# Kernel tuning notes

Hardware: AMD Instinct MI355X
Metric: run time of the kernel (lower is better)

## Reference

```python
import jax, jax.numpy as jnp
import numpy as np

B, NLAY, NX, NXS, NY, NYS, H = 16384, 60, 4, 3, 4, 3, 128


def _lstm(x, h0, c0, Wih, Whh, bih, bhh):
    """torch-style single-layer LSTM (gate order i,f,g,o). x: [B,T,F] -> ([B,T,H], hN, cN)."""
    xs = jnp.swapaxes(x, 0, 1)  # [T,B,F]
    b = bih + bhh

    def step(carry, xt):
        h, c = carry
        z = xt @ Wih.T + h @ Whh.T + b  # [B,4H]
        i, f, g, o = jnp.split(z, 4, axis=-1)
        c = jax.nn.sigmoid(f) * c + jax.nn.sigmoid(i) * jnp.tanh(g)
        h = jax.nn.sigmoid(o) * jnp.tanh(c)
        return (h, c), h

    (hN, cN), hs = jax.lax.scan(step, (h0, c0), xs)
    return jnp.swapaxes(hs, 0, 1), hN, cN


def setup_inputs() -> dict:
    key = jax.random.key(0)
    ks = jax.random.split(key, 23)
    p = lambda k, s: jax.random.normal(k, s, jnp.float32) * 0.05
    nx_rnn1 = NX + H  # nx + nh_mem (memory='Hidden')
    return {
        "inputs_main": jax.random.normal(ks[0], (B, NLAY, NX), jnp.float32),
        "inputs_sfc": jax.random.normal(ks[1], (B, NXS), jnp.float32),
        "rnn1_mem0": jax.random.normal(ks[2], (B, NLAY, H), jnp.float32),
        "hx2": jax.random.normal(ks[3], (B, H), jnp.float32),
        "cx2": jax.random.normal(ks[4], (B, H), jnp.float32),
        "Ws1": p(ks[5], (H, NXS)), "bs1": p(ks[6], (H,)),
        "Ws2": p(ks[7], (H, NXS)), "bs2": p(ks[8], (H,)),
        "Wih1": p(ks[9], (4 * H, nx_rnn1)), "Whh1": p(ks[10], (4 * H, H)),
        "bih1": p(ks[11], (4 * H,)), "bhh1": p(ks[12], (4 * H,)),
        "Wih2": p(ks[13], (4 * H, H)), "Whh2": p(ks[14], (4 * H, H)),
        "bih2": p(ks[15], (4 * H,)), "bhh2": p(ks[16], (4 * H,)),
        "Wlat": p(ks[17], (H, H)), "blat": p(ks[18], (H,)),
        "Wout": p(ks[19], (NY, H)), "bout": p(ks[20], (NY,)),
        "Wsfc": p(ks[21], (NYS, H)), "bsfc": p(ks[22], (NYS,)),
    }


def reference(inputs_main, inputs_sfc, rnn1_mem0, hx2, cx2,
              Ws1, bs1, Ws2, bs2,
              Wih1, Whh1, bih1, bhh1,
              Wih2, Whh2, bih2, bhh2,
              Wlat, blat, Wout, bout, Wsfc, bsfc):
    # initial states for rnn1 from surface features (random_init_cx=False)
    hx = jnp.tanh(inputs_sfc @ Ws1.T + bs1)
    cx = jnp.tanh(inputs_sfc @ Ws2.T + bs2)
    # flip vertical axis (TOA->surface ordering), append hidden memory
    x_flip = inputs_main[:, ::-1, :]
    rnn1_in = jnp.concatenate([x_flip, rnn1_mem0], axis=2)  # [B,NLAY,NX+H]
    r1, _, _ = _lstm(rnn1_in, hx, cx, Wih1, Whh1, bih1, bhh1)
    r1 = r1[:, ::-1, :]  # flip back
    # second LSTM with (externally supplied) random initial states
    r2, hN, _ = _lstm(r1, hx2, cx2, Wih2, Whh2, bih2, bhh2)
    # intermediate mlp + output head (use_intermediate_mlp=True, concat=False)
    lat = r2 @ Wlat.T + blat  # [B,NLAY,H]
    out = lat @ Wout.T + bout  # [B,NLAY,NY]
    out_sfc = hN @ Wsfc.T + bsfc  # [B,NYS]
    return out, out_sfc
```

## Files before the change

### kernel.cpp

```cpp
#include <hip/hip_runtime.h>

#define B_ 16384
#define T_ 60
#define H_ 128
#define LDST 296

typedef unsigned short u16;
typedef short bf16x8 __attribute__((ext_vector_type(8)));
typedef float f32x4 __attribute__((ext_vector_type(4)));

__device__ __forceinline__ u16 f2bf(float f) {
  union { float f; unsigned int u; } v; v.f = f;
  unsigned int r = v.u + 0x7fffu + ((v.u >> 16) & 1u);
  return (u16)(r >> 16);
}
__device__ __forceinline__ float bf2f(u16 b) {
  union { unsigned int u; float f; } v; v.u = ((unsigned int)b) << 16;
  return v.f;
}
__device__ __forceinline__ float sigm(float x) {
  return __builtin_amdgcn_rcpf(1.f + __expf(-x));
}
__device__ __forceinline__ float tanh_f(float x) {
  return 1.f - 2.f * __builtin_amdgcn_rcpf(1.f + __expf(2.f * x));
}

__global__ void prep_kernel(const float* __restrict__ Wih1, const float* __restrict__ Whh1,
                            const float* __restrict__ Wih2, const float* __restrict__ Whh2,
                            const float* __restrict__ Wlat, const float* __restrict__ blat,
                            const float* __restrict__ Wout, const float* __restrict__ bout,
                            u16* __restrict__ wfrag1, u16* __restrict__ wfrag2,
                            float* __restrict__ Wco, float* __restrict__ bco) {
  const int N1 = 9 * 32 * 64;
  const int N2 = 8 * 32 * 64;
  const int total = N1 + N2 + 512 + 4;
  for (int idx = blockIdx.x * blockDim.x + threadIdx.x; idx < total;
       idx += gridDim.x * blockDim.x) {
    if (idx < N1) {
      int c = idx >> 11;
      int rem = idx & 2047;
      int nt = rem >> 6, lane = rem & 63;
      int n = nt * 16 + (lane & 15);
      int kb = c * 32 + (lane >> 4) * 8;
      u16* dst = wfrag1 + (size_t)idx * 8;
      for (int jj = 0; jj < 8; ++jj) {
        int k = kb + jj;
        float x;
        if (k < 128)      x = Wih1[n * 132 + 4 + k];
        else if (k < 256) x = Whh1[n * 128 + (k - 128)];
        else if (k < 260) x = Wih1[n * 132 + (k - 256)];
        else              x = 0.f;
        dst[jj] = f2bf(x);
      }
    } else if (idx < N1 + N2) {
      int i2 = idx - N1;
      int c = i2 >> 11;
      int rem = i2 & 2047;
      int nt = rem >> 6, lane = rem & 63;
      int n = nt * 16 + (lane & 15);
      int kb = c * 32 + (lane >> 4) * 8;
      u16* dst = wfrag2 + (size_t)i2 * 8;
      for (int jj = 0; jj < 8; ++jj) {
        int k = kb + jj;
        float x = (k < 128) ? Wih2[n * 128 + k] : Whh2[n * 128 + (k - 128)];
        dst[jj] = f2bf(x);
      }
    } else if (idx < N1 + N2 + 512) {
      int i = idx - (N1 + N2);
      int y = i >> 7, k = i & 127;
      float acc = 0.f;
      for (int j = 0; j < 128; ++j) acc = fmaf(Wout[y * 128 + j], Wlat[j * 128 + k], acc);
      Wco[i] = acc;
    } else {
      int y = idx - (N1 + N2 + 512);
      float acc = bout[y];
      for (int j = 0; j < 128; ++j) acc = fmaf(Wout[y * 128 + j], blat[j], acc);
      bco[y] = acc;
    }
  }
}

template <int NC>
__device__ __forceinline__ void do_mfma(const u16* __restrict__ As,
                                        const u16* __restrict__ wfrag,
                                        int w, int lane, f32x4 acc[4][4]) {
  const int lr = lane & 15, lq = lane >> 4;
  const u16* ab = As + lr * LDST + lq * 8;
  const u16* bb = wfrag + (size_t)(w * 512 + lane * 8);
  bf16x8 bcur[4];
#pragma unroll
  for (int g = 0; g < 4; ++g) bcur[g] = *(const bf16x8*)(bb + g * 4096);
#pragma unroll
  for (int c = 0; c < NC; ++c) {
    bf16x8 bnxt[4];
    const int cn = (c + 1 < NC) ? c + 1 : c;
#pragma unroll
    for (int g = 0; g < 4; ++g)
      bnxt[g] = *(const bf16x8*)(bb + (size_t)cn * 16384 + g * 4096);
    bf16x8 af[4];
#pragma unroll
    for (int mt = 0; mt < 4; ++mt)
      af[mt] = *(const bf16x8*)(ab + mt * (16 * LDST) + c * 32);
#pragma unroll
    for (int g = 0; g < 4; ++g)
#pragma unroll
      for (int mt = 0; mt < 4; ++mt)
        acc[mt][g] = __builtin_amdgcn_mfma_f32_16x16x32_bf16(af[mt], bcur[g], acc[mt][g], 0, 0, 0);
#pragma unroll
    for (int g = 0; g < 4; ++g) bcur[g] = bnxt[g];
  }
}

__device__ __forceinline__ void cell_update(f32x4 acc[4][4], float4 bz,
                                            float* __restrict__ cr, u16* __restrict__ hb) {
#pragma unroll
  for (int mt = 0; mt < 4; ++mt)
#pragma unroll
    for (int r = 0; r < 4; ++r) {
      int idx = mt * 4 + r;
      float gi = sigm(acc[mt][0][r] + bz.x);
      float gf = sigm(acc[mt][1][r] + bz.y);
      float gg = tanh_f(acc[mt][2][r] + bz.z);
      float go = sigm(acc[mt][3][r] + bz.w);
      float c = gf * cr[idx] + gi * gg;
      cr[idx] = c;
      hb[idx] = f2bf(go * tanh_f(c));
    }
}

__device__ __forceinline__ float dot8w(uint4 hu, const float* __restrict__ wp, float a) {
  const unsigned* h = (const unsigned*)&hu;
#pragma unroll
  for (int i = 0; i < 4; ++i) {
    union { unsigned u; float f; } hl, hh;
    hl.u = h[i] << 16; hh.u = h[i] & 0xffff0000u;
    a = fmaf(hl.f, wp[2 * i], a);
    a = fmaf(hh.f, wp[2 * i + 1], a);
  }
  return a;
}

__global__ __launch_bounds__(512, 2) void rnn_persist(
    const float* __restrict__ inputs_main, const float* __restrict__ inputs_sfc,
    const float* __restrict__ rnn1_mem0, const float* __restrict__ hx2,
    const float* __restrict__ cx2,
    const float* __restrict__ Ws1, const float* __restrict__ bs1,
    const float* __restrict__ Ws2, const float* __restrict__ bs2,
    const float* __restrict__ bih1, const float* __restrict__ bhh1,
    const float* __restrict__ bih2, const float* __restrict__ bhh2,
    const float* __restrict__ Wsfc, const float* __restrict__ bsfc,
    const u16* __restrict__ wfrag1, const u16* __restrict__ wfrag2,
    const float* __restrict__ Wco, const float* __restrict__ bco,
    u16* __restrict__ r1buf, float* __restrict__ out, float* __restrict__ out_sfc) {
  __shared__ __align__(16) u16 As[64 * LDST];
  __shared__ __align__(16) float WcoS[4 * 132];
  __shared__ __align__(16) float WsfcS[3 * 132];

  const int tid = threadIdx.x;
  const int w = tid >> 6, lane = tid & 63, lr = lane & 15, lq = lane >> 4;
  const int jg = w * 16 + lr;
  const size_t row0 = (size_t)blockIdx.x * 64;

  const float4 bz1 = make_float4(bih1[jg] + bhh1[jg], bih1[128 + jg] + bhh1[128 + jg],
                                 bih1[256 + jg] + bhh1[256 + jg], bih1[384 + jg] + bhh1[384 + jg]);
  const float4 bz2 = make_float4(bih2[jg] + bhh2[jg], bih2[128 + jg] + bhh2[128 + jg],
                                 bih2[256 + jg] + bhh2[256 + jg], bih2[384 + jg] + bhh2[384 + jg]);
  const float bcoy = bco[tid & 3];

  if (tid < 512) WcoS[(tid >> 7) * 132 + (tid & 127)] = Wco[tid];
  if (tid < 384) WsfcS[(tid >> 7) * 132 + (tid & 127)] = Wsfc[tid];

#pragma unroll
  for (int kk = 0; kk < 4; ++kk) {
    int f = tid + kk * 512;
    As[(f >> 5) * LDST + 256 + (f & 31)] = 0;
  }

  float cr[16];
  u16 hb[16];
  {
    float w1a = Ws1[jg * 3], w1b = Ws1[jg * 3 + 1], w1c = Ws1[jg * 3 + 2], b1 = bs1[jg];
    float w2a = Ws2[jg * 3], w2b = Ws2[jg * 3 + 1], w2c = Ws2[jg * 3 + 2], b2 = bs2[jg];
#pragma unroll
    for (int mt = 0; mt < 4; ++mt)
#pragma unroll
      for (int r = 0; r < 4; ++r) {
        int rl = mt * 16 + lq * 4 + r;
        const float* sp = inputs_sfc + (row0 + rl) * 3;
        float s0 = sp[0], s1 = sp[1], s2 = sp[2];
        float h0 = tanh_f(fmaf(s2, w1c, fmaf(s1, w1b, fmaf(s0, w1a, b1))));
        cr[mt * 4 + r] = tanh_f(fmaf(s2, w2c, fmaf(s1, w2b, fmaf(s0, w2a, b2))));
        As[rl * LDST + 128 + jg] = f2bf(h0);
      }
  }
#pragma unroll
  for (int kk = 0; kk < 4; ++kk) {
    int f = tid + kk * 512, row = f >> 5, i = f & 31;
    float4 v = *(const float4*)(rnn1_mem0 + (row0 + row) * (T_ * H_) + i * 4);
    *(ushort4*)&As[row * LDST + i * 4] =
        make_ushort4(f2bf(v.x), f2bf(v.y), f2bf(v.z), f2bf(v.w));
  }
  if (tid < 64) {
    float4 v = *(const float4*)(inputs_main + ((row0 + tid) * T_ + 59) * 4);
    *(ushort4*)&As[tid * LDST + 256] = make_ushort4(f2bf(v.x), f2bf(v.y), f2bf(v.z), f2bf(v.w));
  }
  __syncthreads();

#pragma unroll 1
  for (int s = 0; s < T_; ++s) {
    const int sn = (s < 59) ? s + 1 : 59;
    float4 mv[4];
#pragma unroll
    for (int kk = 0; kk < 4; ++kk) {
      int f = tid + kk * 512;
      mv[kk] = *(const float4*)(rnn1_mem0 + (row0 + (f >> 5)) * (T_ * H_) + sn * 128 + (f & 31) * 4);
    }
    float4 xv = make_float4(0, 0, 0, 0);
    if (tid < 64) xv = *(const float4*)(inputs_main + ((row0 + tid) * T_ + (59 - sn)) * 4);

    f32x4 acc[4][4];
#pragma unroll
    for (int mt = 0; mt < 4; ++mt)
#pragma unroll
      for (int g = 0; g < 4; ++g) acc[mt][g] = (f32x4){0.f, 0.f, 0.f, 0.f};
    do_mfma<9>(As, wfrag1, w, lane, acc);
    cell_update(acc, bz1, cr, hb);
#pragma unroll
    for (int mt = 0; mt < 4; ++mt)
#pragma unroll
      for (int r = 0; r < 4; ++r)
        r1buf[((size_t)s * B_ + row0 + mt * 16 + lq * 4 + r) * H_ + jg] = hb[mt * 4 + r];
    __syncthreads();
#pragma unroll
    for (int mt = 0; mt < 4; ++mt)
#pragma unroll
      for (int r = 0; r < 4; ++r)
        As[(mt * 16 + lq * 4 + r) * LDST + 128 + jg] = hb[mt * 4 + r];
#pragma unroll
    for (int kk = 0; kk < 4; ++kk) {
      int f = tid + kk * 512, row = f >> 5, i = f & 31;
      *(ushort4*)&As[row * LDST + i * 4] =
          make_ushort4(f2bf(mv[kk].x), f2bf(mv[kk].y), f2bf(mv[kk].z), f2bf(mv[kk].w));
    }
    if (tid < 64)
      *(ushort4*)&As[tid * LDST + 256] = make_ushort4(f2bf(xv.x), f2bf(xv.y), f2bf(xv.z), f2bf(xv.w));
    __syncthreads();
  }

  {
    uint4 cv[2];
#pragma unroll
    for (int kk = 0; kk < 2; ++kk) {
      int f = tid + kk * 512;
      cv[kk] = *(const uint4*)&As[(f >> 4) * LDST + 128 + (f & 15) * 8];
    }
    __syncthreads();
#pragma unroll
    for (int kk = 0; kk < 2; ++kk) {
      int f = tid + kk * 512;
      *(uint4*)&As[(f >> 4) * LDST + (f & 15) * 8] = cv[kk];
    }
#pragma unroll
    for (int mt = 0; mt < 4; ++mt)
#pragma unroll
      for (int r = 0; r < 4; ++r) {
        int rl = mt * 16 + lq * 4 + r;
        size_t gi = (row0 + rl) * H_ + jg;
        cr[mt * 4 + r] = cx2[gi];
        As[rl * LDST + 128 + jg] = f2bf(hx2[gi]);
      }
    __syncthreads();
  }

#pragma unroll 1
  for (int t = 0; t < T_; ++t) {
    const int slabn = (t < 59) ? (58 - t) : 0;
    uint4 rv[2];
#pragma unroll
    for (int kk = 0; kk < 2; ++kk) {
      int f = tid + kk * 512;
      rv[kk] = *(const uint4*)(r1buf + ((size_t)slabn * B_ + row0 + (f >> 4)) * H_ + (f & 15) * 8);
    }
    f32x4 acc[4][4];
#pragma unroll
    for (int mt = 0; mt < 4; ++mt)
#pragma unroll
      for (int g = 0; g < 4; ++g) acc[mt][g] = (f32x4){0.f, 0.f, 0.f, 0.f};
    do_mfma<8>(As, wfrag2, w, lane, acc);
    cell_update(acc, bz2, cr, hb);
    __syncthreads();
#pragma unroll
    for (int mt = 0; mt < 4; ++mt)
#pragma unroll
      for (int r = 0; r < 4; ++r)
        As[(mt * 16 + lq * 4 + r) * LDST + 128 + jg] = hb[mt * 4 + r];
#pragma unroll
    for (int kk = 0; kk < 2; ++kk) {
      int f = tid + kk * 512;
      *(uint4*)&As[(f >> 4) * LDST + (f & 15) * 8] = rv[kk];
    }
    __syncthreads();
    if (tid < 256) {
      int row = tid >> 2, y = tid & 3;
      float a = bcoy;
      const u16* hrow = As + row * LDST + 128;
      const float* wrow = WcoS + y * 132;
#pragma unroll
      for (int sg = 0; sg < 16; ++sg)
        a = dot8w(*(const uint4*)(hrow + sg * 8), wrow + sg * 8, a);
      out[((row0 + row) * T_ + t) * 4 + y] = a;
    }
    if (t == 59 && tid >= 256) {
      int q = tid - 256;
      int row = q >> 2, y = q & 3;
      if (y < 3) {
        float a = bsfc[y];
        const u16* hrow = As + row * LDST + 128;
        const float* wrow = WsfcS + y * 132;
#pragma unroll
        for (int sg = 0; sg < 16; ++sg)
          a = dot8w(*(const uint4*)(hrow + sg * 8), wrow + sg * 8, a);
        out_sfc[(row0 + row) * 3 + y] = a;
      }
    }
  }
}

extern "C" void kernel_launch(void* const* d_in, const int* in_sizes, int n_in,
                              void* d_out, int out_size, void* d_ws, size_t ws_size,
                              hipStream_t stream) {
  (void)in_sizes; (void)n_in; (void)out_size;
  const float* inputs_main = (const float*)d_in[0];
  const float* inputs_sfc  = (const float*)d_in[1];
  const float* rnn1_mem0   = (const float*)d_in[2];
  const float* hx2         = (const float*)d_in[3];
  const float* cx2         = (const float*)d_in[4];
  const float* Ws1  = (const float*)d_in[5];
  const float* bs1  = (const float*)d_in[6];
  const float* Ws2  = (const float*)d_in[7];
  const float* bs2  = (const float*)d_in[8];
  const float* Wih1 = (const float*)d_in[9];
  const float* Whh1 = (const float*)d_in[10];
  const float* bih1 = (const float*)d_in[11];
  const float* bhh1 = (const float*)d_in[12];
  const float* Wih2 = (const float*)d_in[13];
  const float* Whh2 = (const float*)d_in[14];
  const float* bih2 = (const float*)d_in[15];
  const float* bhh2 = (const float*)d_in[16];
  const float* Wlat = (const float*)d_in[17];
  const float* blat = (const float*)d_in[18];
  const float* Wout = (const float*)d_in[19];
  const float* bout = (const float*)d_in[20];
  const float* Wsfc = (const float*)d_in[21];
  const float* bsfc = (const float*)d_in[22];

  float* out = (float*)d_out;
  float* out_sfc = out + (size_t)B_ * T_ * 4;

  char* p = (char*)d_ws;
  u16* wfrag1 = (u16*)p; p += 294912;
  u16* wfrag2 = (u16*)p; p += 262144;
  float* Wco  = (float*)p; p += 2048;
  float* bco  = (float*)p; p += 64;
  u16* r1buf  = (u16*)p; p += (size_t)T_ * B_ * H_ * 2;
  if ((size_t)(p - (char*)d_ws) > ws_size) return;

  prep_kernel<<<139, 256, 0, stream>>>(Wih1, Whh1, Wih2, Whh2, Wlat, blat, Wout, bout,
                                       wfrag1, wfrag2, Wco, bco);
  rnn_persist<<<256, 512, 0, stream>>>(inputs_main, inputs_sfc, rnn1_mem0, hx2, cx2,
                                       Ws1, bs1, Ws2, bs2,
                                       bih1, bhh1, bih2, bhh2, Wsfc, bsfc,
                                       wfrag1, wfrag2, Wco, bco,
                                       r1buf, out, out_sfc);
}
```

Before: 1.876 ms.

## Keep LSTM weight fragments resident in registers across timesteps

The 8 K-chunks of each LSTM's weight fragments (32 bf16x8 per lane) are now loaded once into registers before each recurrence, so per-step MFMAs no longer reload weights from global memory. Only the small input chunk of layer 1 is still read each step. The per-element r1buf stores become coalesced 16-byte copies of the previous step's h read back from LDS, and one bias register is reused for both layers. The extra 128 VGPRs per lane raise register pressure and may cause spills or lower occupancy.

Result: faster. 1.582 ms (-15.7%).

```diff
diff --git a/kernel.cpp b/kernel.cpp
--- a/kernel.cpp
+++ b/kernel.cpp
@@ -80,35 +80,49 @@
   }
 }
 
-template <int NC>
-__device__ __forceinline__ void do_mfma(const u16* __restrict__ As,
-                                        const u16* __restrict__ wfrag,
-                                        int w, int lane, f32x4 acc[4][4]) {
+__device__ __forceinline__ void mfma_x(const u16* __restrict__ As, const bf16x8 bx[4],
+                                       int lane, f32x4 acc[4][4]) {
   const int lr = lane & 15, lq = lane >> 4;
   const u16* ab = As + lr * LDST + lq * 8;
+  bf16x8 af[4];
+#pragma unroll
+  for (int mt = 0; mt < 4; ++mt)
+    af[mt] = *(const bf16x8*)(ab + mt * (16 * LDST) + 256);
+#pragma unroll
+  for (int g = 0; g < 4; ++g)
+#pragma unroll
+    for (int mt = 0; mt < 4; ++mt)
+      acc[mt][g] = __builtin_amdgcn_mfma_f32_16x16x32_bf16(af[mt], bx[g], acc[mt][g], 0, 0, 0);
+}
+
+template <int NC>
+__device__ __forceinline__ void mfma_w(const u16* __restrict__ As,
+                                       const bf16x8* __restrict__ wreg,
+                                       int lane, f32x4 acc[4][4]) {
+  const int lr = lane & 15, lq = lane >> 4;
+  const u16* ab = As + lr * LDST + lq * 8;
+#pragma unroll
+  for (int c = 0; c < NC; ++c) {
+    bf16x8 af[4];
+#pragma unroll
+    for (int mt = 0; mt < 4; ++mt)
+      af[mt] = *(const bf16x8*)(ab + mt * (16 * LDST) + c * 32);
+#pragma unroll
+    for (int g = 0; g < 4; ++g)
+#pragma unroll
+      for (int mt = 0; mt < 4; ++mt)
+        acc[mt][g] = __builtin_amdgcn_mfma_f32_16x16x32_bf16(af[mt], wreg[c * 4 + g], acc[mt][g], 0, 0, 0);
+  }
+}
+
+__device__ __forceinline__ void load_wreg(const u16* __restrict__ wfrag, int w, int lane,
+                                          bf16x8* __restrict__ wreg) {
   const u16* bb = wfrag + (size_t)(w * 512 + lane * 8);
-  bf16x8 bcur[4];
-#pragma unroll
-  for (int g = 0; g < 4; ++g) bcur[g] = *(const bf16x8*)(bb + g * 4096);
-#pragma unroll
-  for (int c = 0; c < NC; ++c) {
-    bf16x8 bnxt[4];
-    const int cn = (c + 1 < NC) ? c + 1 : c;
+#pragma unroll
+  for (int c = 0; c < 8; ++c)
 #pragma unroll
     for (int g = 0; g < 4; ++g)
-      bnxt[g] = *(const bf16x8*)(bb + (size_t)cn * 16384 + g * 4096);
-    bf16x8 af[4];
-#pragma unroll
-    for (int mt = 0; mt < 4; ++mt)
-      af[mt] = *(const bf16x8*)(ab + mt * (16 * LDST) + c * 32);
-#pragma unroll
-    for (int g = 0; g < 4; ++g)
-#pragma unroll
-      for (int mt = 0; mt < 4; ++mt)
-        acc[mt][g] = __builtin_amdgcn_mfma_f32_16x16x32_bf16(af[mt], bcur[g], acc[mt][g], 0, 0, 0);
-#pragma unroll
-    for (int g = 0; g < 4; ++g) bcur[g] = bnxt[g];
-  }
+      wreg[c * 4 + g] = *(const bf16x8*)(bb + (size_t)c * 16384 + g * 4096);
 }
 
 __device__ __forceinline__ void cell_update(f32x4 acc[4][4], float4 bz,
@@ -161,10 +175,8 @@
   const int jg = w * 16 + lr;
   const size_t row0 = (size_t)blockIdx.x * 64;
 
-  const float4 bz1 = make_float4(bih1[jg] + bhh1[jg], bih1[128 + jg] + bhh1[128 + jg],
-                                 bih1[256 + jg] + bhh1[256 + jg], bih1[384 + jg] + bhh1[384 + jg]);
-  const float4 bz2 = make_float4(bih2[jg] + bhh2[jg], bih2[128 + jg] + bhh2[128 + jg],
-                                 bih2[256 + jg] + bhh2[256 + jg], bih2[384 + jg] + bhh2[384 + jg]);
+  float4 bz = make_float4(bih1[jg] + bhh1[jg], bih1[128 + jg] + bhh1[128 + jg],
+                          bih1[256 + jg] + bhh1[256 + jg], bih1[384 + jg] + bhh1[384 + jg]);
   const float bcoy = bco[tid & 3];
 
   if (tid < 512) WcoS[(tid >> 7) * 132 + (tid & 127)] = Wco[tid];
@@ -175,6 +187,10 @@
     int f = tid + kk * 512;
     As[(f >> 5) * LDST + 256 + (f & 31)] = 0;
   }
+
+  bf16x8 wreg[32];
+  load_wreg(wfrag1, w, lane, wreg);
+  const u16* bxp = wfrag1 + (size_t)(w * 512 + lane * 8) + (size_t)8 * 16384;
 
   float cr[16];
   u16 hb[16];
@@ -208,6 +224,26 @@
 
 #pragma unroll 1
   for (int s = 0; s < T_; ++s) {
+    if (s > 0) {
+#pragma unroll
+      for (int kk = 0; kk < 2; ++kk) {
+        int f = tid + kk * 512;
+        uint4 hv = *(const uint4*)&As[(f >> 4) * LDST + 128 + (f & 15) * 8];
+        *(uint4*)(r1buf + ((size_t)(s - 1) * B_ + row0 + (f >> 4)) * H_ + (f & 15) * 8) = hv;
+      }
+    }
+    bf16x8 bx[4];
+#pragma unroll
+    for (int g = 0; g < 4; ++g) bx[g] = *(const bf16x8*)(bxp + g * 4096);
+
+    f32x4 acc[4][4];
+#pragma unroll
+    for (int mt = 0; mt < 4; ++mt)
+#pragma unroll
+      for (int g = 0; g < 4; ++g) acc[mt][g] = (f32x4){0.f, 0.f, 0.f, 0.f};
+    mfma_x(As, bx, lane, acc);
+    mfma_w<8>(As, wreg, lane, acc);
+
     const int sn = (s < 59) ? s + 1 : 59;
     float4 mv[4];
 #pragma unroll
@@ -218,18 +254,7 @@
     float4 xv = make_float4(0, 0, 0, 0);
     if (tid < 64) xv = *(const float4*)(inputs_main + ((row0 + tid) * T_ + (59 - sn)) * 4);
 
-    f32x4 acc[4][4];
-#pragma unroll
-    for (int mt = 0; mt < 4; ++mt)
-#pragma unroll
-      for (int g = 0; g < 4; ++g) acc[mt][g] = (f32x4){0.f, 0.f, 0.f, 0.f};
-    do_mfma<9>(As, wfrag1, w, lane, acc);
-    cell_update(acc, bz1, cr, hb);
-#pragma unroll
-    for (int mt = 0; mt < 4; ++mt)
-#pragma unroll
-      for (int r = 0; r < 4; ++r)
-        r1buf[((size_t)s * B_ + row0 + mt * 16 + lq * 4 + r) * H_ + jg] = hb[mt * 4 + r];
+    cell_update(acc, bz, cr, hb);
     __syncthreads();
 #pragma unroll
     for (int mt = 0; mt < 4; ++mt)
@@ -254,6 +279,9 @@
       int f = tid + kk * 512;
       cv[kk] = *(const uint4*)&As[(f >> 4) * LDST + 128 + (f & 15) * 8];
     }
+    bz = make_float4(bih2[jg] + bhh2[jg], bih2[128 + jg] + bhh2[128 + jg],
+                     bih2[256 + jg] + bhh2[256 + jg], bih2[384 + jg] + bhh2[384 + jg]);
+    load_wreg(wfrag2, w, lane, wreg);
     __syncthreads();
 #pragma unroll
     for (int kk = 0; kk < 2; ++kk) {
@@ -286,8 +314,8 @@
     for (int mt = 0; mt < 4; ++mt)
 #pragma unroll
       for (int g = 0; g < 4; ++g) acc[mt][g] = (f32x4){0.f, 0.f, 0.f, 0.f};
-    do_mfma<8>(As, wfrag2, w, lane, acc);
-    cell_update(acc, bz2, cr, hb);
+    mfma_w<8>(As, wreg, lane, acc);
+    cell_update(acc, bz, cr, hb);
     __syncthreads();
 #pragma unroll
     for (int mt = 0; mt < 4; ++mt)
```
